# Kernel optimization log

Measured on AMD Instinct MI355X. Metric: run time of the kernel, lower is better.

Reference implementation:

```python
import jax, jax.numpy as jnp
import numpy as np

N_NODES = 100000
HIDDEN = 128
N_EDGES = 1600000


def setup_inputs() -> dict:
    key = jax.random.key(0)
    k_z, k_e, k_w1, k_b1, k_w2, k_b2 = jax.random.split(key, 6)
    z = jax.random.normal(k_z, (N_NODES, HIDDEN), dtype=jnp.float32)
    edge_index = jax.random.randint(k_e, (2, N_EDGES), 0, N_NODES, dtype=jnp.int64)
    # torch.nn.Linear default init: U(-1/sqrt(fan_in), 1/sqrt(fan_in))
    lim1 = 1.0 / np.sqrt(2 * HIDDEN)
    W1 = jax.random.uniform(k_w1, (2 * HIDDEN, HIDDEN), minval=-lim1, maxval=lim1, dtype=jnp.float32)
    b1 = jax.random.uniform(k_b1, (HIDDEN,), minval=-lim1, maxval=lim1, dtype=jnp.float32)
    lim2 = 1.0 / np.sqrt(HIDDEN)
    W2 = jax.random.uniform(k_w2, (HIDDEN, 1), minval=-lim2, maxval=lim2, dtype=jnp.float32)
    b2 = jax.random.uniform(k_b2, (1,), minval=-lim2, maxval=lim2, dtype=jnp.float32)
    return {"z": z, "edge_index": edge_index, "W1": W1, "b1": b1, "W2": W2, "b2": b2}


def reference(z, edge_index, W1, b1, W2, b2):
    src = edge_index[0]
    dst = edge_index[1]
    # gather node pairs -> concat: [E, 2H]
    edge_feat = jnp.concatenate([z[src], z[dst]], axis=1)
    h = jax.nn.relu(edge_feat @ W1 + b1)  # [E, H]
    score = h @ W2 + b2                   # [E, 1]
    return score
```

## Files before the change

kernel.cpp:

```cpp
#include <hip/hip_runtime.h>
#include <hip/hip_bf16.h>
#include <stdint.h>

#define HIDDEN 128
#define EPG 8
#define NBLK_SORT 256
#define NBUK 256

typedef __attribute__((ext_vector_type(8))) short bf16x8;
typedef __attribute__((ext_vector_type(16))) float f32x16;

static __device__ __forceinline__ uint32_t cvt2(float a, float b) {
    union { __hip_bfloat162 h2; uint32_t u; } c;
    c.h2 = __float22bfloat162_rn(make_float2(a, b));
    return c.u;
}
static __device__ __forceinline__ float bf_lo(uint32_t p) {
    union { uint32_t u; float f; } v; v.u = p << 16; return v.f;
}
static __device__ __forceinline__ float bf_hi(uint32_t p) {
    union { uint32_t u; float f; } v; v.u = p & 0xffff0000u; return v.f;
}

__global__ __launch_bounds__(256) void transpose_w1(
    const float* __restrict__ W1, unsigned short* __restrict__ Wt)
{
    const int t = blockIdx.x * 256 + threadIdx.x;
    if (t >= 4096) return;
    const int cc = t >> 4;
    const int kg = t & 15;
    const int ccol = cc & 127;
    const int kofs = (cc >= 128) ? 128 : 0;
    uint32_t u[4];
    #pragma unroll
    for (int p = 0; p < 4; ++p) {
        const float a = W1[(size_t)(kofs + kg * 8 + 2 * p) * 128 + ccol];
        const float b = W1[(size_t)(kofs + kg * 8 + 2 * p + 1) * 128 + ccol];
        u[p] = cvt2(a, b);
    }
    uint4 o = { u[0], u[1], u[2], u[3] };
    *reinterpret_cast<uint4*>(Wt + (size_t)cc * 128 + kg * 8) = o;
}

__global__ __launch_bounds__(256) void precompute_mfma32(
    const float* __restrict__ z, const float* __restrict__ W1,
    const unsigned short* __restrict__ Wt,
    unsigned short* __restrict__ UV, int n_nodes, int n_groups)
{
    __shared__ char Zt[32 * 256];
    __shared__ char Sm[32 * 512];

    const int tid = threadIdx.x;
    const int lane = tid & 63;
    const int w = tid >> 6;
    const int nl = lane & 31;
    const int hi = lane >> 5;

    const int st_node = tid >> 3;
    const int st_j2 = tid & 7;
    const int st_swz = (st_node & 7) << 4;
    const int st_addrA = st_node * 256 + ((st_j2 * 32) ^ st_swz);
    const int st_addrB = st_node * 256 + ((st_j2 * 32 + 16) ^ st_swz);

    bf16x8 wf[2][8];
    if (Wt) {
        #pragma unroll
        for (int cg = 0; cg < 2; ++cg) {
            const int cc = w * 64 + cg * 32 + nl;
            #pragma unroll
            for (int ks = 0; ks < 8; ++ks)
                wf[cg][ks] = *reinterpret_cast<const bf16x8*>(
                    Wt + (size_t)cc * 128 + ks * 16 + hi * 8);
        }
    } else {
        #pragma unroll
        for (int cg = 0; cg < 2; ++cg) {
            const int cc = w * 64 + cg * 32 + nl;
            const int ccol = cc & 127;
            const int kofs = (cc >= 128) ? 128 : 0;
            #pragma unroll
            for (int ks = 0; ks < 8; ++ks) {
                const int k0 = ks * 16 + hi * 8 + kofs;
                float t[8];
                #pragma unroll
                for (int j = 0; j < 8; ++j)
                    t[j] = W1[(size_t)(k0 + j) * 128 + ccol];
                union { uint32_t u[4]; bf16x8 v; } fu;
                fu.u[0] = cvt2(t[0], t[1]); fu.u[1] = cvt2(t[2], t[3]);
                fu.u[2] = cvt2(t[4], t[5]); fu.u[3] = cvt2(t[6], t[7]);
                wf[cg][ks] = fu.v;
            }
        }
    }

    const int stride = gridDim.x;
    int ng = blockIdx.x;
    if (ng >= n_groups) return;

    float4 nz0, nz1, nz2, nz3;
    {
        int node = ng * 32 + st_node;
        node = (node < n_nodes) ? node : (n_nodes - 1);
        const float* zp = z + (size_t)node * HIDDEN + st_j2 * 16;
        nz0 = *reinterpret_cast<const float4*>(zp);
        nz1 = *reinterpret_cast<const float4*>(zp + 4);
        nz2 = *reinterpret_cast<const float4*>(zp + 8);
        nz3 = *reinterpret_cast<const float4*>(zp + 12);
    }

    while (ng < n_groups) {
        {
            uint4 A, B;
            A.x = cvt2(nz0.x, nz0.y); A.y = cvt2(nz0.z, nz0.w);
            A.z = cvt2(nz1.x, nz1.y); A.w = cvt2(nz1.z, nz1.w);
            B.x = cvt2(nz2.x, nz2.y); B.y = cvt2(nz2.z, nz2.w);
            B.z = cvt2(nz3.x, nz3.y); B.w = cvt2(nz3.z, nz3.w);
            *reinterpret_cast<uint4*>(Zt + st_addrA) = A;
            *reinterpret_cast<uint4*>(Zt + st_addrB) = B;
        }

        const int ngn = ng + stride;
        if (ngn < n_groups) {
            int node = ngn * 32 + st_node;
            node = (node < n_nodes) ? node : (n_nodes - 1);
            const float* zp = z + (size_t)node * HIDDEN + st_j2 * 16;
            nz0 = *reinterpret_cast<const float4*>(zp);
            nz1 = *reinterpret_cast<const float4*>(zp + 4);
            nz2 = *reinterpret_cast<const float4*>(zp + 8);
            nz3 = *reinterpret_cast<const float4*>(zp + 12);
        }

        __syncthreads();

        {
            const int rd_swz = (nl & 7) << 4;
            bf16x8 zf[8];
            #pragma unroll
            for (int ks = 0; ks < 8; ++ks) {
                const int off = ks * 32 + hi * 16;
                zf[ks] = *reinterpret_cast<const bf16x8*>(
                    Zt + nl * 256 + (off ^ rd_swz));
            }

            f32x16 acc0 = {};
            f32x16 acc1 = {};
            #pragma unroll
            for (int ks = 0; ks < 8; ++ks) {
                acc0 = __builtin_amdgcn_mfma_f32_32x32x16_bf16(wf[0][ks], zf[ks], acc0, 0, 0, 0);
                acc1 = __builtin_amdgcn_mfma_f32_32x32x16_bf16(wf[1][ks], zf[ks], acc1, 0, 0, 0);
            }

            const int swz = (nl & 15) << 3;
            #pragma unroll
            for (int g = 0; g < 4; ++g) {
                uint2 s0, s1;
                s0.x = cvt2(acc0[4 * g + 0], acc0[4 * g + 1]);
                s0.y = cvt2(acc0[4 * g + 2], acc0[4 * g + 3]);
                s1.x = cvt2(acc1[4 * g + 0], acc1[4 * g + 1]);
                s1.y = cvt2(acc1[4 * g + 2], acc1[4 * g + 3]);
                const int colb0 = w * 128 + g * 16 + hi * 8;
                const int colb1 = w * 128 + 64 + g * 16 + hi * 8;
                *reinterpret_cast<uint2*>(Sm + nl * 512 + (colb0 ^ swz)) = s0;
                *reinterpret_cast<uint2*>(Sm + nl * 512 + (colb1 ^ swz)) = s1;
            }
        }

        __syncthreads();

        {
            const int colb0 = (tid & 31) * 16;
            #pragma unroll
            for (int rep = 0; rep < 4; ++rep) {
                const int node_local = rep * 8 + (tid >> 5);
                const int swz = (node_local & 15) << 3;
                const uint2 g0 = *reinterpret_cast<const uint2*>(Sm + node_local * 512 + ((colb0) ^ swz));
                const uint2 g1 = *reinterpret_cast<const uint2*>(Sm + node_local * 512 + ((colb0 + 8) ^ swz));
                const int node = ng * 32 + node_local;
                if (node < n_nodes) {
                    uint4 o = { g0.x, g0.y, g1.x, g1.y };
                    *reinterpret_cast<uint4*>(UV + (size_t)node * 256 + (tid & 31) * 8) = o;
                }
            }
        }

        ng = ngn;
    }
}

__global__ __launch_bounds__(256) void hist2(
    const int* __restrict__ ei, int* __restrict__ h,
    int n_edges, int chunk, int sh)
{
    __shared__ int lh[NBUK];
    const int t = threadIdx.x;
    if (t < NBUK) lh[t] = 0;
    __syncthreads();
    const int e0 = blockIdx.x * chunk;
    const int e1 = min(e0 + chunk, n_edges);
    for (int e = e0 + t; e < e1; e += 256)
        atomicAdd(&lh[((unsigned)ei[e]) >> sh], 1);
    __syncthreads();
    if (t < NBUK) h[t * NBLK_SORT + blockIdx.x] = lh[t];
}

__global__ __launch_bounds__(1024) void scan2(int* __restrict__ h)
{
    __shared__ int s[1024];
    const int t = threadIdx.x;
    int sum = 0;
    for (int i = 0; i < 64; ++i) sum += h[t * 64 + i];
    s[t] = sum;
    __syncthreads();
    for (int d = 1; d < 1024; d <<= 1) {
        const int x = (t >= d) ? s[t - d] : 0;
        __syncthreads();
        s[t] += x;
        __syncthreads();
    }
    int run = s[t] - sum;
    for (int i = 0; i < 64; ++i) {
        const int idx = t * 64 + i;
        const int v = h[idx];
        h[idx] = run;
        run += v;
    }
}

__global__ __launch_bounds__(256) void scatter2(
    const int* __restrict__ ei, const int* __restrict__ gscan,
    int2* __restrict__ sd, int* __restrict__ inv,
    int n_edges, int chunk, int sh)
{
    __shared__ int lbase[NBUK];
    __shared__ int lrank[NBUK];
    const int t = threadIdx.x;
    if (t < NBUK) {
        lbase[t] = gscan[t * NBLK_SORT + blockIdx.x];
        lrank[t] = 0;
    }
    __syncthreads();
    const int e0 = blockIdx.x * chunk;
    const int e1 = min(e0 + chunk, n_edges);
    for (int e = e0 + t; e < e1; e += 256) {
        const int s = ei[e];
        const int d = ei[n_edges + e];
        const int b = ((unsigned)s) >> sh;
        const int r = atomicAdd(&lrank[b], 1);
        const int pos = lbase[b] + r;
        sd[pos] = make_int2(s, d);
        inv[e] = pos;
    }
}

__global__ __launch_bounds__(256) void permute_out(
    const float* __restrict__ tmp, const int* __restrict__ inv,
    float* __restrict__ out, int n_edges)
{
    const int e0 = (blockIdx.x * 256 + threadIdx.x) * 4;
    if (e0 + 3 < n_edges) {
        const int4 iv = *reinterpret_cast<const int4*>(inv + e0);
        float4 o = { tmp[iv.x], tmp[iv.y], tmp[iv.z], tmp[iv.w] };
        *reinterpret_cast<float4*>(out + e0) = o;
    } else {
        for (int i = 0; i < 4; ++i) {
            const int e = e0 + i;
            if (e < n_edges) out[e] = tmp[inv[e]];
        }
    }
}

static __device__ __forceinline__ float dot8(uint4 u, uint4 v,
                                             const float* w, const float* bb) {
    const uint32_t up[4] = { u.x, u.y, u.z, u.w };
    const uint32_t vp[4] = { v.x, v.y, v.z, v.w };
    float s = 0.f;
    #pragma unroll
    for (int p = 0; p < 4; ++p) {
        const float h0 = bf_lo(up[p]) + bf_lo(vp[p]) + bb[2 * p];
        const float h1 = bf_hi(up[p]) + bf_hi(vp[p]) + bb[2 * p + 1];
        s = fmaf(fmaxf(h0, 0.f), w[2 * p], s);
        s = fmaf(fmaxf(h1, 0.f), w[2 * p + 1], s);
    }
    return s;
}
static __device__ __forceinline__ float red16(float s) {
    s += __shfl_xor(s, 1, 64); s += __shfl_xor(s, 2, 64);
    s += __shfl_xor(s, 4, 64); s += __shfl_xor(s, 8, 64);
    return s;
}

template <int PACKED>
__global__ __launch_bounds__(256, 4) void edge_score_t(
    const int2* __restrict__ sd,
    const int* __restrict__ srcp, const int* __restrict__ dstp,
    const unsigned short* __restrict__ UV,
    const float* __restrict__ b1, const float* __restrict__ W2,
    const float* __restrict__ b2, float* __restrict__ outp, int n_edges)
{
    int vb = blockIdx.x;
    if (PACKED) {
        const int nb = gridDim.x;
        const int q8 = nb >> 3, r8 = nb & 7;
        const int x = blockIdx.x & 7, i = blockIdx.x >> 3;
        vb = (x < r8 ? x * (q8 + 1) : r8 * (q8 + 1) + (x - r8) * q8) + i;
    }

    const int g = (vb * 256 + (int)threadIdx.x) >> 4;
    const int q = threadIdx.x & 15;
    const int e0 = g * EPG;
    if (e0 >= n_edges) return;

    const float4 w2a = *reinterpret_cast<const float4*>(W2 + q * 8);
    const float4 w2b = *reinterpret_cast<const float4*>(W2 + q * 8 + 4);
    const float wloc[8] = { w2a.x, w2a.y, w2a.z, w2a.w, w2b.x, w2b.y, w2b.z, w2b.w };
    const float4 b1a = *reinterpret_cast<const float4*>(b1 + q * 8);
    const float4 b1b = *reinterpret_cast<const float4*>(b1 + q * 8 + 4);
    const float bb[8] = { b1a.x, b1a.y, b1a.z, b1a.w, b1b.x, b1b.y, b1b.z, b1b.w };
    const float bias = b2[0];

    const char* UVb = (const char*)UV;
    const uint32_t qo = (uint32_t)q * 16u;

    if (e0 + EPG - 1 < n_edges) {
        int sidx[EPG], didx[EPG];
        if (PACKED) {
            const int4 p0 = *reinterpret_cast<const int4*>(sd + e0);
            const int4 p1 = *reinterpret_cast<const int4*>(sd + e0 + 2);
            const int4 p2 = *reinterpret_cast<const int4*>(sd + e0 + 4);
            const int4 p3 = *reinterpret_cast<const int4*>(sd + e0 + 6);
            sidx[0]=p0.x; didx[0]=p0.y; sidx[1]=p0.z; didx[1]=p0.w;
            sidx[2]=p1.x; didx[2]=p1.y; sidx[3]=p1.z; didx[3]=p1.w;
            sidx[4]=p2.x; didx[4]=p2.y; sidx[5]=p2.z; didx[5]=p2.w;
            sidx[6]=p3.x; didx[6]=p3.y; sidx[7]=p3.z; didx[7]=p3.w;
        } else {
            const int4 sA = *reinterpret_cast<const int4*>(srcp + e0);
            const int4 sB = *reinterpret_cast<const int4*>(srcp + e0 + 4);
            const int4 dA = *reinterpret_cast<const int4*>(dstp + e0);
            const int4 dB = *reinterpret_cast<const int4*>(dstp + e0 + 4);
            sidx[0]=sA.x; sidx[1]=sA.y; sidx[2]=sA.z; sidx[3]=sA.w;
            sidx[4]=sB.x; sidx[5]=sB.y; sidx[6]=sB.z; sidx[7]=sB.w;
            didx[0]=dA.x; didx[1]=dA.y; didx[2]=dA.z; didx[3]=dA.w;
            didx[4]=dB.x; didx[5]=dB.y; didx[6]=dB.z; didx[7]=dB.w;
        }

        uint4 u[EPG], v[EPG];
        #pragma unroll
        for (int ii = 0; ii < EPG; ++ii) {
            u[ii] = *reinterpret_cast<const uint4*>(UVb + ((uint32_t)sidx[ii] * 512u + qo));
            v[ii] = *reinterpret_cast<const uint4*>(UVb + ((uint32_t)didx[ii] * 512u + 256u + qo));
        }
        __builtin_amdgcn_sched_barrier(0);

        float s[EPG];
        #pragma unroll
        for (int ii = 0; ii < EPG; ++ii) s[ii] = dot8(u[ii], v[ii], wloc, bb);
        #pragma unroll
        for (int ii = 0; ii < EPG; ++ii) s[ii] = red16(s[ii]) + bias;

        if (q == 0) {
            float4 oA = { s[0], s[1], s[2], s[3] };
            float4 oB = { s[4], s[5], s[6], s[7] };
            *reinterpret_cast<float4*>(outp + e0) = oA;
            *reinterpret_cast<float4*>(outp + e0 + 4) = oB;
        }
    } else {
        for (int ii = 0; ii < EPG; ++ii) {
            const int e = e0 + ii;
            if (e >= n_edges) break;
            const int si = PACKED ? sd[e].x : srcp[e];
            const int di = PACKED ? sd[e].y : dstp[e];
            const uint4 uu = *reinterpret_cast<const uint4*>(UVb + ((uint32_t)si * 512u + qo));
            const uint4 vv = *reinterpret_cast<const uint4*>(UVb + ((uint32_t)di * 512u + 256u + qo));
            float s = red16(dot8(uu, vv, wloc, bb));
            if (q == 0) outp[e] = s + bias;
        }
    }
}

extern "C" void kernel_launch(void* const* d_in, const int* in_sizes, int n_in,
                              void* d_out, int out_size, void* d_ws, size_t ws_size,
                              hipStream_t stream) {
    const float* z  = (const float*)d_in[0];
    const int*   ei = (const int*)d_in[1];
    const float* W1 = (const float*)d_in[2];
    const float* b1 = (const float*)d_in[3];
    const float* W2 = (const float*)d_in[4];
    const float* b2 = (const float*)d_in[5];
    float* out = (float*)d_out;

    const int n_nodes = in_sizes[0] / HIDDEN;
    const int n_edges = in_sizes[1] / 2;

    int sh = 0;
    while (((unsigned)(n_nodes - 1) >> sh) >= NBUK) sh++;

    char* wsp = (char*)d_ws;
    size_t off = 0;
    auto alloc = [&](size_t bytes) -> char* {
        char* p = wsp + off;
        off = (off + bytes + 255) & ~(size_t)255;
        return p;
    };
    unsigned short* UV = (unsigned short*)alloc((size_t)n_nodes * 256 * 2);
    unsigned short* Wt = (unsigned short*)alloc(256 * 128 * 2);
    const size_t base_need = off;
    int*  h    = (int*)alloc((size_t)NBUK * NBLK_SORT * 4);
    int2* sd   = (int2*)alloc((size_t)n_edges * 8);
    int*  inv  = (int*)alloc((size_t)n_edges * 4);
    float* tmp = (float*)alloc((size_t)n_edges * 4);
    const bool have_wt = ws_size >= base_need;
    const bool do_sort = ws_size >= off;

    if (have_wt) transpose_w1<<<16, 256, 0, stream>>>(W1, Wt);

    {
        const int n_groups = (n_nodes + 31) / 32;
        const int g1 = n_groups < 768 ? n_groups : 768;
        precompute_mfma32<<<g1, 256, 0, stream>>>(z, W1, have_wt ? Wt : nullptr,
                                                  UV, n_nodes, n_groups);
    }

    const int groups = (n_edges + EPG - 1) / EPG;
    const int eblocks = (groups * 16 + 255) / 256;

    if (do_sort) {
        const int chunk = (n_edges + NBLK_SORT - 1) / NBLK_SORT;
        hist2<<<NBLK_SORT, 256, 0, stream>>>(ei, h, n_edges, chunk, sh);
        scan2<<<1, 1024, 0, stream>>>(h);
        scatter2<<<NBLK_SORT, 256, 0, stream>>>(ei, h, sd, inv, n_edges, chunk, sh);
        edge_score_t<1><<<eblocks, 256, 0, stream>>>(sd, nullptr, nullptr, UV,
                                                     b1, W2, b2, tmp, n_edges);
        const int pblocks = ((n_edges + 3) / 4 + 255) / 256;
        permute_out<<<pblocks, 256, 0, stream>>>(tmp, inv, out, n_edges);
    } else {
        edge_score_t<0><<<eblocks, 256, 0, stream>>>(nullptr, ei, ei + n_edges, UV,
                                                     b1, W2, b2, out, n_edges);
    }
}
```

Measured before the change: 146.9 us.

## Scatter scores directly to original positions and parallelize bucket scan

The single-block serial scan over the 256x256 histogram is replaced by a two-level parallel scan (per-row scans in 256 blocks plus a small scan of row totals). The scatter kernel now records each sorted slot's original edge index, and the edge scoring kernel writes each score straight to its original output position. This removes the separate permute_out kernel and the temporary score buffer. The cost is that output writes become scattered 4-byte stores instead of coalesced float4 stores, and there is one extra small kernel launch.

```diff
diff --git a/kernel.cpp b/kernel.cpp
--- a/kernel.cpp
+++ b/kernel.cpp
@@ -203,39 +203,51 @@
     if (t < NBUK) h[t * NBLK_SORT + blockIdx.x] = lh[t];
 }
 
-__global__ __launch_bounds__(1024) void scan2(int* __restrict__ h)
-{
-    __shared__ int s[1024];
+__global__ __launch_bounds__(NBLK_SORT) void scanP1(
+    int* __restrict__ h, int* __restrict__ rowtot)
+{
+    __shared__ int s[NBLK_SORT];
+    const int b = blockIdx.x, t = threadIdx.x;
+    const int v = h[b * NBLK_SORT + t];
+    s[t] = v;
+    __syncthreads();
+    for (int d = 1; d < NBLK_SORT; d <<= 1) {
+        const int x = (t >= d) ? s[t - d] : 0;
+        __syncthreads();
+        s[t] += x;
+        __syncthreads();
+    }
+    h[b * NBLK_SORT + t] = s[t] - v;
+    if (t == NBLK_SORT - 1) rowtot[b] = s[t];
+}
+
+__global__ __launch_bounds__(NBUK) void scanP2(int* __restrict__ rowtot)
+{
+    __shared__ int s[NBUK];
     const int t = threadIdx.x;
-    int sum = 0;
-    for (int i = 0; i < 64; ++i) sum += h[t * 64 + i];
-    s[t] = sum;
+    const int v = rowtot[t];
+    s[t] = v;
     __syncthreads();
-    for (int d = 1; d < 1024; d <<= 1) {
+    for (int d = 1; d < NBUK; d <<= 1) {
         const int x = (t >= d) ? s[t - d] : 0;
         __syncthreads();
         s[t] += x;
         __syncthreads();
     }
-    int run = s[t] - sum;
-    for (int i = 0; i < 64; ++i) {
-        const int idx = t * 64 + i;
-        const int v = h[idx];
-        h[idx] = run;
-        run += v;
-    }
+    rowtot[t] = s[t] - v;
 }
 
 __global__ __launch_bounds__(256) void scatter2(
-    const int* __restrict__ ei, const int* __restrict__ gscan,
-    int2* __restrict__ sd, int* __restrict__ inv,
+    const int* __restrict__ ei, const int* __restrict__ h,
+    const int* __restrict__ base,
+    int2* __restrict__ sd, int* __restrict__ org,
     int n_edges, int chunk, int sh)
 {
     __shared__ int lbase[NBUK];
     __shared__ int lrank[NBUK];
     const int t = threadIdx.x;
     if (t < NBUK) {
-        lbase[t] = gscan[t * NBLK_SORT + blockIdx.x];
+        lbase[t] = h[t * NBLK_SORT + blockIdx.x] + base[t];
         lrank[t] = 0;
     }
     __syncthreads();
@@ -248,24 +260,7 @@
         const int r = atomicAdd(&lrank[b], 1);
         const int pos = lbase[b] + r;
         sd[pos] = make_int2(s, d);
-        inv[e] = pos;
-    }
-}
-
-__global__ __launch_bounds__(256) void permute_out(
-    const float* __restrict__ tmp, const int* __restrict__ inv,
-    float* __restrict__ out, int n_edges)
-{
-    const int e0 = (blockIdx.x * 256 + threadIdx.x) * 4;
-    if (e0 + 3 < n_edges) {
-        const int4 iv = *reinterpret_cast<const int4*>(inv + e0);
-        float4 o = { tmp[iv.x], tmp[iv.y], tmp[iv.z], tmp[iv.w] };
-        *reinterpret_cast<float4*>(out + e0) = o;
-    } else {
-        for (int i = 0; i < 4; ++i) {
-            const int e = e0 + i;
-            if (e < n_edges) out[e] = tmp[inv[e]];
-        }
+        org[pos] = e;
     }
 }
 
@@ -291,7 +286,7 @@
 
 template <int PACKED>
 __global__ __launch_bounds__(256, 4) void edge_score_t(
-    const int2* __restrict__ sd,
+    const int2* __restrict__ sd, const int* __restrict__ org,
     const int* __restrict__ srcp, const int* __restrict__ dstp,
     const unsigned short* __restrict__ UV,
     const float* __restrict__ b1, const float* __restrict__ W2,
@@ -358,10 +353,19 @@
         for (int ii = 0; ii < EPG; ++ii) s[ii] = red16(s[ii]) + bias;
 
         if (q == 0) {
-            float4 oA = { s[0], s[1], s[2], s[3] };
-            float4 oB = { s[4], s[5], s[6], s[7] };
-            *reinterpret_cast<float4*>(outp + e0) = oA;
-            *reinterpret_cast<float4*>(outp + e0 + 4) = oB;
+            if (PACKED) {
+                const int4 o0 = *reinterpret_cast<const int4*>(org + e0);
+                const int4 o1 = *reinterpret_cast<const int4*>(org + e0 + 4);
+                outp[o0.x] = s[0]; outp[o0.y] = s[1];
+                outp[o0.z] = s[2]; outp[o0.w] = s[3];
+                outp[o1.x] = s[4]; outp[o1.y] = s[5];
+                outp[o1.z] = s[6]; outp[o1.w] = s[7];
+            } else {
+                float4 oA = { s[0], s[1], s[2], s[3] };
+                float4 oB = { s[4], s[5], s[6], s[7] };
+                *reinterpret_cast<float4*>(outp + e0) = oA;
+                *reinterpret_cast<float4*>(outp + e0 + 4) = oB;
+            }
         }
     } else {
         for (int ii = 0; ii < EPG; ++ii) {
@@ -372,7 +376,10 @@
             const uint4 uu = *reinterpret_cast<const uint4*>(UVb + ((uint32_t)si * 512u + qo));
             const uint4 vv = *reinterpret_cast<const uint4*>(UVb + ((uint32_t)di * 512u + 256u + qo));
             float s = red16(dot8(uu, vv, wloc, bb));
-            if (q == 0) outp[e] = s + bias;
+            if (q == 0) {
+                if (PACKED) outp[org[e]] = s + bias;
+                else        outp[e] = s + bias;
+            }
         }
     }
 }
@@ -404,10 +411,10 @@
     unsigned short* UV = (unsigned short*)alloc((size_t)n_nodes * 256 * 2);
     unsigned short* Wt = (unsigned short*)alloc(256 * 128 * 2);
     const size_t base_need = off;
-    int*  h    = (int*)alloc((size_t)NBUK * NBLK_SORT * 4);
-    int2* sd   = (int2*)alloc((size_t)n_edges * 8);
-    int*  inv  = (int*)alloc((size_t)n_edges * 4);
-    float* tmp = (float*)alloc((size_t)n_edges * 4);
+    int*  h      = (int*)alloc((size_t)NBUK * NBLK_SORT * 4);
+    int*  rowtot = (int*)alloc((size_t)NBUK * 4);
+    int2* sd     = (int2*)alloc((size_t)n_edges * 8);
+    int*  org    = (int*)alloc((size_t)n_edges * 4);
     const bool have_wt = ws_size >= base_need;
     const bool do_sort = ws_size >= off;
 
@@ -426,14 +433,14 @@
     if (do_sort) {
         const int chunk = (n_edges + NBLK_SORT - 1) / NBLK_SORT;
         hist2<<<NBLK_SORT, 256, 0, stream>>>(ei, h, n_edges, chunk, sh);
-        scan2<<<1, 1024, 0, stream>>>(h);
-        scatter2<<<NBLK_SORT, 256, 0, stream>>>(ei, h, sd, inv, n_edges, chunk, sh);
-        edge_score_t<1><<<eblocks, 256, 0, stream>>>(sd, nullptr, nullptr, UV,
-                                                     b1, W2, b2, tmp, n_edges);
-        const int pblocks = ((n_edges + 3) / 4 + 255) / 256;
-        permute_out<<<pblocks, 256, 0, stream>>>(tmp, inv, out, n_edges);
+        scanP1<<<NBUK, NBLK_SORT, 0, stream>>>(h, rowtot);
+        scanP2<<<1, NBUK, 0, stream>>>(rowtot);
+        scatter2<<<NBLK_SORT, 256, 0, stream>>>(ei, h, rowtot, sd, org,
+                                                n_edges, chunk, sh);
+        edge_score_t<1><<<eblocks, 256, 0, stream>>>(sd, org, nullptr, nullptr, UV,
+                                                     b1, W2, b2, out, n_edges);
     } else {
-        edge_score_t<0><<<eblocks, 256, 0, stream>>>(nullptr, ei, ei + n_edges, UV,
-                                                     b1, W2, b2, out, n_edges);
-    }
-}
+        edge_score_t<0><<<eblocks, 256, 0, stream>>>(nullptr, nullptr, ei, ei + n_edges,
+                                                     UV, b1, W2, b2, out, n_edges);
+    }
+}
```

Result: faster. 133.6 us (-9.0%).
